# Kernel optimization log

Measured on AMD Instinct MI355X. Metric: run time of the kernel, lower is better.

## Reference

```python
import jax, jax.numpy as jnp
import numpy as np

N_NODES = 30000
N_EDGES = 480000
IN_CH, NF, OUT_CH = 64, 128, 3
N_HIDDEN = 6  # GCN(num_layers=7): conv0 (in->nf) + 6 convs (nf->nf)
SLOPE = 0.02


def setup_inputs() -> dict:
    key = jax.random.key(0)
    ks = jax.random.split(key, 8)
    x = jax.random.normal(ks[0], (N_NODES, IN_CH), dtype=jnp.float32)
    edge_index = jax.random.randint(ks[1], (2, N_EDGES), 0, N_NODES, dtype=jnp.int64)
    W0 = jax.random.normal(ks[2], (IN_CH, NF), dtype=jnp.float32) * (1.0 / np.sqrt(IN_CH))
    b0 = jnp.zeros((NF,), dtype=jnp.float32)
    Wh = jax.random.normal(ks[3], (N_HIDDEN, NF, NF), dtype=jnp.float32) * (1.0 / np.sqrt(NF))
    bh = jnp.zeros((N_HIDDEN, NF), dtype=jnp.float32)
    Wout = jax.random.normal(ks[4], (NF, OUT_CH), dtype=jnp.float32) * (1.0 / np.sqrt(NF))
    bout = jnp.zeros((OUT_CH,), dtype=jnp.float32)
    return {"x": x, "edge_index": edge_index, "W0": W0, "b0": b0,
            "Wh": Wh, "bh": bh, "Wout": Wout, "bout": bout}


def _gcn_norm(edge_index, n):
    # PyG GCNConv default: add self-loops, symmetric normalization D^-1/2 (A+I) D^-1/2
    loop = jnp.arange(n, dtype=edge_index.dtype)
    src = jnp.concatenate([edge_index[0], loop])
    dst = jnp.concatenate([edge_index[1], loop])
    deg = jax.ops.segment_sum(jnp.ones_like(dst, dtype=jnp.float32), dst, num_segments=n)
    dinv = jax.lax.rsqrt(deg)  # deg >= 1 due to self-loops
    norm = dinv[src] * dinv[dst]  # [E+N]
    return src, dst, norm


def _gcn_conv(h, W, b, src, dst, norm, n):
    h = h @ W                                   # [N, F_out]
    msg = h[src] * norm[:, None]                # gather + scale  [E+N, F_out]
    out = jax.ops.segment_sum(msg, dst, num_segments=n)  # scatter-add
    return out + b


def reference(x, edge_index, W0, b0, Wh, bh, Wout, bout):
    n = x.shape[0]
    src, dst, norm = _gcn_norm(edge_index, n)
    # 7-layer GCN stack with LeakyReLU(0.02) between layers; dropout is
    # identity in eval mode (training=False).
    h = _gcn_conv(x, W0, b0, src, dst, norm, n)
    for i in range(N_HIDDEN):
        h = jax.nn.leaky_relu(h, SLOPE)
        h = _gcn_conv(h, Wh[i], bh[i], src, dst, norm, n)
    # outer forward: leaky_relu -> dropout(eval=identity) -> out conv -> tanh*0.5
    h = jax.nn.leaky_relu(h, SLOPE)
    h = _gcn_conv(h, Wout, bout, src, dst, norm, n)
    return jnp.tanh(h) * 0.5
```

## Files before the change

### kernel.cpp

```cpp
#include <hip/hip_runtime.h>
#include <hip/hip_fp16.h>
#include <math.h>

#define NN 30000
#define NE 480000
#define NB 118
#define SCALE 512.0f
#define INVSCALE (1.0f / 512.0f)

typedef _Float16 half8 __attribute__((ext_vector_type(8)));
typedef float floatx4 __attribute__((ext_vector_type(4)));

__device__ __forceinline__ float lrelu(float v) { return v > 0.0f ? v : v * 0.02f; }

__device__ __forceinline__ float4 fma4(float4 v, float w, float4 a) {
    a.x = fmaf(v.x, w, a.x);
    a.y = fmaf(v.y, w, a.y);
    a.z = fmaf(v.z, w, a.z);
    a.w = fmaf(v.w, w, a.w);
    return a;
}

__device__ __forceinline__ float4 loadh4(const __half* p) {
    uint2 raw = *(const uint2*)p;
    float2 f0 = __half22float2(*(__half2*)&raw.x);
    float2 f1 = __half22float2(*(__half2*)&raw.y);
    return make_float4(f0.x, f0.y, f1.x, f1.y);
}

__device__ __forceinline__ void loadh8(const __half* p, float4* lo, float4* hi) {
    uint4 raw = *(const uint4*)p;
    float2 f0 = __half22float2(*(__half2*)&raw.x);
    float2 f1 = __half22float2(*(__half2*)&raw.y);
    float2 f2 = __half22float2(*(__half2*)&raw.z);
    float2 f3 = __half22float2(*(__half2*)&raw.w);
    *lo = make_float4(f0.x, f0.y, f1.x, f1.y);
    *hi = make_float4(f2.x, f2.y, f3.x, f3.y);
}

__device__ __forceinline__ void stnt_h(__half* p, float v) {
    __half hh = __float2half(v);
    __builtin_nontemporal_store(*(_Float16*)&hh, (_Float16*)p);
}


__global__ void k_count(const int* __restrict__ ei, int* __restrict__ cnt,
                        const float* __restrict__ W0, const float* __restrict__ Wh,
                        const float* __restrict__ b0, const float* __restrict__ bh,
                        const float* __restrict__ x,
                        __half* __restrict__ W0t, __half* __restrict__ Wht,
                        float* __restrict__ bs, __half* __restrict__ x16) {
    int g = blockIdx.x * 256 + threadIdx.x;
    if (g < NE) atomicAdd(&cnt[ei[NE + g]], 1);
    {
        float4 v = *(const float4*)&x[(size_t)g * 4];
        __half2 a = __floats2half2_rn(v.x, v.y);
        __half2 b = __floats2half2_rn(v.z, v.w);
        uint2 pk;
        pk.x = *(unsigned int*)&a;
        pk.y = *(unsigned int*)&b;
        *(uint2*)&x16[(size_t)g * 4] = pk;
    }
    if (g < 8192) {
        int k = g >> 7, n = g & 127;
        W0t[n * 64 + k] = __float2half(W0[g] * SCALE);
    } else if (g < 8192 + 98304) {
        int j = g - 8192;
        int l = j >> 14;
        int r = j & 16383;
        int k = r >> 7, n = r & 127;
        Wht[l * 16384 + n * 128 + k] = __float2half(Wh[j]);
    } else if (g < 8192 + 98304 + 896) {
        int j = g - 8192 - 98304;
        bs[j] = (j < 128 ? b0[j] : bh[j - 128]) * SCALE;
    }
}

__global__ void k_scan1(const int* __restrict__ cnt, int* __restrict__ bsum,
                        float* __restrict__ dinv) {
    __shared__ int sd[256];
    int tid = threadIdx.x;
    int i = blockIdx.x * 256 + tid;
    int v = (i < NN) ? cnt[i] : 0;
    if (i < NN) dinv[i] = 1.0f / sqrtf((float)(v + 1));
    sd[tid] = v;
    __syncthreads();
    for (int off = 128; off > 0; off >>= 1) {
        if (tid < off) sd[tid] += sd[tid + off];
        __syncthreads();
    }
    if (tid == 0) bsum[blockIdx.x] = sd[0];
}

__global__ void k_scan3(const int* __restrict__ cnt, const int* __restrict__ bsum,
                        int* __restrict__ row_ptr, int* __restrict__ cursor) {
    __shared__ int sd[256];
    __shared__ int offs[128];
    int tid = threadIdx.x;
    if (tid < 128) offs[tid] = (tid < blockIdx.x) ? bsum[tid] : 0;
    __syncthreads();
    for (int o = 64; o > 0; o >>= 1) {
        if (tid < o) offs[tid] += offs[tid + o];
        __syncthreads();
    }
    int i = blockIdx.x * 256 + tid;
    int v = (i < NN) ? cnt[i] : 0;
    sd[tid] = v;
    __syncthreads();
    for (int off = 1; off < 256; off <<= 1) {
        int t = (tid >= off) ? sd[tid - off] : 0;
        __syncthreads();
        sd[tid] += t;
        __syncthreads();
    }
    if (i < NN) {
        int excl = offs[0] + sd[tid] - v;
        row_ptr[i] = excl;
        cursor[i] = excl;
        if (i == NN - 1) row_ptr[NN] = excl + v;
    }
}

__global__ void k_fill(const int* __restrict__ ei, const float* __restrict__ dinv,
                       int* __restrict__ cursor, int2* __restrict__ csr) {
    int e = blockIdx.x * 256 + threadIdx.x;
    if (e < NE) {
        int s = ei[e];
        int d = ei[NE + e];
        int pos = atomicAdd(&cursor[d], 1);
        float w = dinv[s] * dinv[d];
        csr[pos] = make_int2(s, __float_as_int(w));
    }
}


__launch_bounds__(256)
__global__ void k_layer0(const __half* __restrict__ x, const int* __restrict__ row_ptr,
                         const int2* __restrict__ csr, const float* __restrict__ dinv,
                         const __half* __restrict__ Wt, const float* __restrict__ bias,
                         __half* __restrict__ out16) {
    __shared__ _Float16 hsF[2 * 4 * 16 * 8];
    int tid = threadIdx.x;
    int node0 = blockIdx.x * 16;
    {
        int nl = tid >> 4;
        int node = node0 + nl;
        int c = (tid & 15) * 4;
        float di = dinv[node];
        float w0 = di * di;
        float4 hv = loadh4(&x[(size_t)node * 64 + c]);
        float4 acc[8];
        acc[0] = make_float4(hv.x * w0, hv.y * w0, hv.z * w0, hv.w * w0);
        #pragma unroll
        for (int j = 1; j < 8; j++) acc[j] = make_float4(0.f, 0.f, 0.f, 0.f);
        int e = row_ptr[node];
        int e1 = row_ptr[node + 1];
        for (; e + 8 <= e1; e += 8) {
            int2 sw[8];
            #pragma unroll
            for (int j = 0; j < 8; j++) sw[j] = csr[e + j];
            float4 v[8];
            #pragma unroll
            for (int j = 0; j < 8; j++) v[j] = loadh4(&x[(size_t)sw[j].x * 64 + c]);
            #pragma unroll
            for (int j = 0; j < 8; j++) acc[j] = fma4(v[j], __int_as_float(sw[j].y), acc[j]);
        }
        for (; e < e1; ++e) {
            int2 sw = csr[e];
            float4 v = loadh4(&x[(size_t)sw.x * 64 + c]);
            acc[0] = fma4(v, __int_as_float(sw.y), acc[0]);
        }
        #pragma unroll
        for (int j = 1; j < 8; j++) {
            acc[0].x += acc[j].x;
            acc[0].y += acc[j].y;
            acc[0].z += acc[j].z;
            acc[0].w += acc[j].w;
        }
        int ks = c >> 5, quad = (c >> 3) & 3, jj = c & 7;
        __half2 p0 = __floats2half2_rn(acc[0].x, acc[0].y);
        __half2 p1 = __floats2half2_rn(acc[0].z, acc[0].w);
        uint2 pk;
        pk.x = *(unsigned int*)&p0;
        pk.y = *(unsigned int*)&p1;
        *(uint2*)&hsF[((ks * 4 + quad) * 16 + nl) * 8 + jj] = pk;
    }
    __syncthreads();
    int wave = tid >> 6, lane = tid & 63, quad = lane >> 4, ln = lane & 15;
    half8 afrag[2];
    #pragma unroll
    for (int ks = 0; ks < 2; ks++)
        afrag[ks] = *(const half8*)&hsF[((ks * 4 + quad) * 16 + ln) * 8];
    #pragma unroll
    for (int tc = 0; tc < 2; tc++) {
        int tt = wave + tc * 4;
        floatx4 acc = (floatx4){0.f, 0.f, 0.f, 0.f};
        #pragma unroll
        for (int ks = 0; ks < 2; ks++) {
            half8 b = *(const half8*)&Wt[(size_t)(tt * 16 + ln) * 64 + ks * 32 + quad * 8];
            acc = __builtin_amdgcn_mfma_f32_16x16x32_f16(afrag[ks], b, acc, 0, 0, 0);
        }
        int col = tt * 16 + ln;
        float bb = bias[col];
        #pragma unroll
        for (int r = 0; r < 4; r++) {
            int row = node0 + quad * 4 + r;
            stnt_h(&out16[(size_t)row * 128 + col], lrelu(acc[r] + bb));
        }
    }
}

template <bool LAST>
__launch_bounds__(256)
__global__ void k_layer_h(const __half* __restrict__ h, const int* __restrict__ row_ptr,
                          const int2* __restrict__ csr, const float* __restrict__ dinv,
                          const __half* __restrict__ Wt, const float* __restrict__ bias,
                          __half* __restrict__ out16, const float* __restrict__ Wout,
                          float* __restrict__ u) {
    __shared__ _Float16 hsF[4 * 4 * 16 * 8];
    __shared__ float uacc[4][16][3];
    int tid = threadIdx.x;
    int node0 = blockIdx.x * 16;
    {
        int nl = tid >> 4;
        int node = node0 + nl;
        int c = (tid & 15) * 8;
        float di = dinv[node];
        float w0 = di * di;
        float4 hlo, hhi;
        loadh8(&h[(size_t)node * 128 + c], &hlo, &hhi);
        float4 acc[4][2];
        acc[0][0] = make_float4(hlo.x * w0, hlo.y * w0, hlo.z * w0, hlo.w * w0);
        acc[0][1] = make_float4(hhi.x * w0, hhi.y * w0, hhi.z * w0, hhi.w * w0);
        #pragma unroll
        for (int j = 1; j < 4; j++) {
            acc[j][0] = make_float4(0.f, 0.f, 0.f, 0.f);
            acc[j][1] = make_float4(0.f, 0.f, 0.f, 0.f);
        }
        int e = row_ptr[node];
        int e1 = row_ptr[node + 1];
        for (; e + 4 <= e1; e += 4) {
            int2 sw[4];
            #pragma unroll
            for (int j = 0; j < 4; j++) sw[j] = csr[e + j];
            float4 vlo[4], vhi[4];
            #pragma unroll
            for (int j = 0; j < 4; j++)
                loadh8(&h[(size_t)sw[j].x * 128 + c], &vlo[j], &vhi[j]);
            #pragma unroll
            for (int j = 0; j < 4; j++) {
                float w = __int_as_float(sw[j].y);
                acc[j][0] = fma4(vlo[j], w, acc[j][0]);
                acc[j][1] = fma4(vhi[j], w, acc[j][1]);
            }
        }
        for (; e < e1; ++e) {
            int2 sw = csr[e];
            float4 vlo, vhi;
            loadh8(&h[(size_t)sw.x * 128 + c], &vlo, &vhi);
            float w = __int_as_float(sw.y);
            acc[0][0] = fma4(vlo, w, acc[0][0]);
            acc[0][1] = fma4(vhi, w, acc[0][1]);
        }
        #pragma unroll
        for (int j = 1; j < 4; j++) {
            acc[0][0].x += acc[j][0].x; acc[0][0].y += acc[j][0].y;
            acc[0][0].z += acc[j][0].z; acc[0][0].w += acc[j][0].w;
            acc[0][1].x += acc[j][1].x; acc[0][1].y += acc[j][1].y;
            acc[0][1].z += acc[j][1].z; acc[0][1].w += acc[j][1].w;
        }
        int ks = c >> 5, quad = (c >> 3) & 3;
        __half2 p0 = __floats2half2_rn(acc[0][0].x, acc[0][0].y);
        __half2 p1 = __floats2half2_rn(acc[0][0].z, acc[0][0].w);
        __half2 p2 = __floats2half2_rn(acc[0][1].x, acc[0][1].y);
        __half2 p3 = __floats2half2_rn(acc[0][1].z, acc[0][1].w);
        uint4 pk;
        pk.x = *(unsigned int*)&p0;
        pk.y = *(unsigned int*)&p1;
        pk.z = *(unsigned int*)&p2;
        pk.w = *(unsigned int*)&p3;
        *(uint4*)&hsF[((ks * 4 + quad) * 16 + nl) * 8] = pk;
    }
    __syncthreads();
    int wave = tid >> 6, lane = tid & 63, quad = lane >> 4, ln = lane & 15;
    half8 afrag[4];
    #pragma unroll
    for (int ks = 0; ks < 4; ks++)
        afrag[ks] = *(const half8*)&hsF[((ks * 4 + quad) * 16 + ln) * 8];

    float up[4][3];
    if (LAST) {
        #pragma unroll
        for (int r = 0; r < 4; r++)
            #pragma unroll
            for (int cc = 0; cc < 3; cc++) up[r][cc] = 0.f;
    }

    #pragma unroll
    for (int tc = 0; tc < 2; tc++) {
        int tt = wave + tc * 4;
        floatx4 acc = (floatx4){0.f, 0.f, 0.f, 0.f};
        #pragma unroll
        for (int ks = 0; ks < 4; ks++) {
            half8 b = *(const half8*)&Wt[(size_t)(tt * 16 + ln) * 128 + ks * 32 + quad * 8];
            acc = __builtin_amdgcn_mfma_f32_16x16x32_f16(afrag[ks], b, acc, 0, 0, 0);
        }
        int col = tt * 16 + ln;
        float bb = bias[col];
        if (LAST) {
            float w0o = Wout[col * 3 + 0];
            float w1o = Wout[col * 3 + 1];
            float w2o = Wout[col * 3 + 2];
            #pragma unroll
            for (int r = 0; r < 4; r++) {
                float hv = __half2float(__float2half(lrelu(acc[r] + bb)));
                up[r][0] = fmaf(hv, w0o, up[r][0]);
                up[r][1] = fmaf(hv, w1o, up[r][1]);
                up[r][2] = fmaf(hv, w2o, up[r][2]);
            }
        } else {
            #pragma unroll
            for (int r = 0; r < 4; r++) {
                int row = node0 + quad * 4 + r;
                stnt_h(&out16[(size_t)row * 128 + col], lrelu(acc[r] + bb));
            }
        }
    }

    if (LAST) {
        #pragma unroll
        for (int m = 1; m < 16; m <<= 1) {
            #pragma unroll
            for (int r = 0; r < 4; r++) {
                #pragma unroll
                for (int cc = 0; cc < 3; cc++)
                    up[r][cc] += __shfl_xor(up[r][cc], m);
            }
        }
        if (ln == 0) {
            #pragma unroll
            for (int r = 0; r < 4; r++) {
                #pragma unroll
                for (int cc = 0; cc < 3; cc++)
                    uacc[wave][quad * 4 + r][cc] = up[r][cc];
            }
        }
        __syncthreads();
        if (tid < 48) {
            int row = tid / 3, cc = tid % 3;
            float s = (uacc[0][row][cc] + uacc[1][row][cc]) +
                      (uacc[2][row][cc] + uacc[3][row][cc]);
            u[(size_t)(node0 + row) * 3 + cc] = s;
        }
    }
}


__global__ void k_agg_out(const float* __restrict__ u, const int* __restrict__ row_ptr,
                          const int2* __restrict__ csr, const float* __restrict__ dinv,
                          const float* __restrict__ bout, float* __restrict__ out) {
    int node = blockIdx.x * 256 + threadIdx.x;
    if (node >= NN) return;
    float di = dinv[node], w0 = di * di;
    float s0 = u[(size_t)node * 3 + 0] * w0;
    float s1 = u[(size_t)node * 3 + 1] * w0;
    float s2 = u[(size_t)node * 3 + 2] * w0;
    float b0a = 0.f, b1a = 0.f, b2a = 0.f;
    int e = row_ptr[node];
    int e1 = row_ptr[node + 1];
    for (; e + 2 <= e1; e += 2) {
        int2 swa = csr[e], swb = csr[e + 1];
        float wa = __int_as_float(swa.y), wb = __int_as_float(swb.y);
        const float* ua = &u[(size_t)swa.x * 3];
        const float* ub = &u[(size_t)swb.x * 3];
        s0 = fmaf(ua[0], wa, s0);
        s1 = fmaf(ua[1], wa, s1);
        s2 = fmaf(ua[2], wa, s2);
        b0a = fmaf(ub[0], wb, b0a);
        b1a = fmaf(ub[1], wb, b1a);
        b2a = fmaf(ub[2], wb, b2a);
    }
    for (; e < e1; ++e) {
        int2 sw = csr[e];
        float w = __int_as_float(sw.y);
        const float* us = &u[(size_t)sw.x * 3];
        s0 = fmaf(us[0], w, s0);
        s1 = fmaf(us[1], w, s1);
        s2 = fmaf(us[2], w, s2);
    }
    out[(size_t)node * 3 + 0] = tanhf((s0 + b0a) * INVSCALE + bout[0]) * 0.5f;
    out[(size_t)node * 3 + 1] = tanhf((s1 + b1a) * INVSCALE + bout[1]) * 0.5f;
    out[(size_t)node * 3 + 2] = tanhf((s2 + b2a) * INVSCALE + bout[2]) * 0.5f;
}


extern "C" void kernel_launch(void* const* d_in, const int* in_sizes, int n_in,
                              void* d_out, int out_size, void* d_ws, size_t ws_size,
                              hipStream_t stream) {
    const float* x        = (const float*)d_in[0];
    const int*   ei       = (const int*)d_in[1];
    const float* W0       = (const float*)d_in[2];
    const float* b0       = (const float*)d_in[3];
    const float* Wh       = (const float*)d_in[4];
    const float* bh       = (const float*)d_in[5];
    const float* Wout     = (const float*)d_in[6];
    const float* bout     = (const float*)d_in[7];
    float* out            = (float*)d_out;

    char* ws = (char*)d_ws;
    float*  bufA   = (float*)(ws + 0);
    __half* bufB16 = (__half*)(ws + 15360000);
    __half* bufC16 = (__half*)(ws + 23040000);
    __half* x16    = (__half*)(ws + 30720000);
    __half* W0t16  = (__half*)(ws + 34560000);
    __half* Wht16  = (__half*)(ws + 34576384);
    float*  bs     = (float*)(ws + 34772992);
    float*  dinv   = (float*)(ws + 34776576);
    int*    cnt    = (int*)  (ws + 34896576);
    int*    row_ptr= (int*)  (ws + 35016576);
    int*    cursor = (int*)  (ws + 35136640);
    int2*   csr    = (int2*) (ws + 35256640);

    int* bsum = (int*)bufA;

    hipMemsetAsync(cnt, 0, NN * sizeof(int), stream);
    k_count<<<(NE + 255) / 256, 256, 0, stream>>>(ei, cnt, W0, Wh, b0, bh, x,
                                                  W0t16, Wht16, bs, x16);
    k_scan1<<<NB, 256, 0, stream>>>(cnt, bsum, dinv);
    k_scan3<<<NB, 256, 0, stream>>>(cnt, bsum, row_ptr, cursor);
    k_fill<<<(NE + 255) / 256, 256, 0, stream>>>(ei, dinv, cursor, csr);

    k_layer0<<<NN / 16, 256, 0, stream>>>(x16, row_ptr, csr, dinv, W0t16, bs, bufB16);

    __half* hin = bufB16;
    __half* hout = bufC16;
    for (int i = 0; i < 5; i++) {
        k_layer_h<false><<<NN / 16, 256, 0, stream>>>(hin, row_ptr, csr, dinv,
                                                      Wht16 + (size_t)i * 16384,
                                                      bs + 128 + (size_t)i * 128, hout,
                                                      Wout, bufA);
        __half* t = hin; hin = hout; hout = t;
    }
    k_layer_h<true><<<NN / 16, 256, 0, stream>>>(hin, row_ptr, csr, dinv,
                                                 Wht16 + (size_t)5 * 16384,
                                                 bs + 128 + (size_t)5 * 128, hout,
                                                 Wout, bufA );

    k_agg_out<<<(NN + 255) / 256, 256, 0, stream>>>(bufA, row_ptr, csr, dinv, bout, out);
}
```

Baseline: 316.5 us.

## Sort nodes by degree via counting-sort permutation to balance aggregation work

Builds a 64-bin in-degree histogram and a counting-sort permutation of nodes. Each layer kernel and the output aggregation then process nodes in degree order, so the 16 nodes in a block have similar edge counts and threads in a wave diverge less. The cost is an extra indirection through perm on reads and writes, scattered output stores, a serial single-thread prefix over 64 bins in scan3, and global atomics in scan1 and fill. Indexing u, out16 and out through perm keeps results in original node order.

After: 469.3 us. 48.3% more time.

```diff
diff --git a/kernel.cpp b/kernel.cpp
--- a/kernel.cpp
+++ b/kernel.cpp
@@ -77,12 +77,15 @@
 }
 
 __global__ void k_scan1(const int* __restrict__ cnt, int* __restrict__ bsum,
-                        float* __restrict__ dinv) {
+                        float* __restrict__ dinv, int* __restrict__ hist) {
     __shared__ int sd[256];
     int tid = threadIdx.x;
     int i = blockIdx.x * 256 + tid;
     int v = (i < NN) ? cnt[i] : 0;
-    if (i < NN) dinv[i] = 1.0f / sqrtf((float)(v + 1));
+    if (i < NN) {
+        dinv[i] = 1.0f / sqrtf((float)(v + 1));
+        atomicAdd(&hist[v < 63 ? v : 63], 1);
+    }
     sd[tid] = v;
     __syncthreads();
     for (int off = 128; off > 0; off >>= 1) {
@@ -93,7 +96,12 @@
 }
 
 __global__ void k_scan3(const int* __restrict__ cnt, const int* __restrict__ bsum,
-                        int* __restrict__ row_ptr, int* __restrict__ cursor) {
+                        int* __restrict__ row_ptr, int* __restrict__ cursor,
+                        const int* __restrict__ hist, int* __restrict__ cursor2) {
+    if (blockIdx.x == 0 && threadIdx.x == 0) {
+        int run = 0;
+        for (int d = 0; d < 64; d++) { cursor2[d] = run; run += hist[d]; }
+    }
     __shared__ int sd[256];
     __shared__ int offs[128];
     int tid = threadIdx.x;
@@ -122,7 +130,9 @@
 }
 
 __global__ void k_fill(const int* __restrict__ ei, const float* __restrict__ dinv,
-                       int* __restrict__ cursor, int2* __restrict__ csr) {
+                       int* __restrict__ cursor, int2* __restrict__ csr,
+                       const int* __restrict__ cnt, int* __restrict__ cursor2,
+                       int* __restrict__ perm) {
     int e = blockIdx.x * 256 + threadIdx.x;
     if (e < NE) {
         int s = ei[e];
@@ -131,6 +141,11 @@
         float w = dinv[s] * dinv[d];
         csr[pos] = make_int2(s, __float_as_int(w));
     }
+    if (e < NN) {
+        int dg = cnt[e];
+        int p = atomicAdd(&cursor2[dg < 63 ? dg : 63], 1);
+        perm[p] = e;
+    }
 }
 
 
@@ -138,13 +153,13 @@
 __global__ void k_layer0(const __half* __restrict__ x, const int* __restrict__ row_ptr,
                          const int2* __restrict__ csr, const float* __restrict__ dinv,
                          const __half* __restrict__ Wt, const float* __restrict__ bias,
-                         __half* __restrict__ out16) {
+                         __half* __restrict__ out16, const int* __restrict__ perm) {
     __shared__ _Float16 hsF[2 * 4 * 16 * 8];
     int tid = threadIdx.x;
     int node0 = blockIdx.x * 16;
     {
         int nl = tid >> 4;
-        int node = node0 + nl;
+        int node = perm[node0 + nl];
         int c = (tid & 15) * 4;
         float di = dinv[node];
         float w0 = di * di;
@@ -191,6 +206,9 @@
     #pragma unroll
     for (int ks = 0; ks < 2; ks++)
         afrag[ks] = *(const half8*)&hsF[((ks * 4 + quad) * 16 + ln) * 8];
+    int rn[4];
+    #pragma unroll
+    for (int r = 0; r < 4; r++) rn[r] = perm[node0 + quad * 4 + r];
     #pragma unroll
     for (int tc = 0; tc < 2; tc++) {
         int tt = wave + tc * 4;
@@ -203,10 +221,8 @@
         int col = tt * 16 + ln;
         float bb = bias[col];
         #pragma unroll
-        for (int r = 0; r < 4; r++) {
-            int row = node0 + quad * 4 + r;
-            stnt_h(&out16[(size_t)row * 128 + col], lrelu(acc[r] + bb));
-        }
+        for (int r = 0; r < 4; r++)
+            stnt_h(&out16[(size_t)rn[r] * 128 + col], lrelu(acc[r] + bb));
     }
 }
 
@@ -216,14 +232,14 @@
                           const int2* __restrict__ csr, const float* __restrict__ dinv,
                           const __half* __restrict__ Wt, const float* __restrict__ bias,
                           __half* __restrict__ out16, const float* __restrict__ Wout,
-                          float* __restrict__ u) {
+                          float* __restrict__ u, const int* __restrict__ perm) {
     __shared__ _Float16 hsF[4 * 4 * 16 * 8];
     __shared__ float uacc[4][16][3];
     int tid = threadIdx.x;
     int node0 = blockIdx.x * 16;
     {
         int nl = tid >> 4;
-        int node = node0 + nl;
+        int node = perm[node0 + nl];
         int c = (tid & 15) * 8;
         float di = dinv[node];
         float w0 = di * di;
@@ -295,6 +311,9 @@
             #pragma unroll
             for (int cc = 0; cc < 3; cc++) up[r][cc] = 0.f;
     }
+    int rn[4];
+    #pragma unroll
+    for (int r = 0; r < 4; r++) rn[r] = perm[node0 + quad * 4 + r];
 
     #pragma unroll
     for (int tc = 0; tc < 2; tc++) {
@@ -320,10 +339,8 @@
             }
         } else {
             #pragma unroll
-            for (int r = 0; r < 4; r++) {
-                int row = node0 + quad * 4 + r;
-                stnt_h(&out16[(size_t)row * 128 + col], lrelu(acc[r] + bb));
-            }
+            for (int r = 0; r < 4; r++)
+                stnt_h(&out16[(size_t)rn[r] * 128 + col], lrelu(acc[r] + bb));
         }
     }
 
@@ -350,7 +367,7 @@
             int row = tid / 3, cc = tid % 3;
             float s = (uacc[0][row][cc] + uacc[1][row][cc]) +
                       (uacc[2][row][cc] + uacc[3][row][cc]);
-            u[(size_t)(node0 + row) * 3 + cc] = s;
+            u[(size_t)perm[node0 + row] * 3 + cc] = s;
         }
     }
 }
@@ -358,9 +375,11 @@
 
 __global__ void k_agg_out(const float* __restrict__ u, const int* __restrict__ row_ptr,
                           const int2* __restrict__ csr, const float* __restrict__ dinv,
-                          const float* __restrict__ bout, float* __restrict__ out) {
-    int node = blockIdx.x * 256 + threadIdx.x;
-    if (node >= NN) return;
+                          const float* __restrict__ bout, float* __restrict__ out,
+                          const int* __restrict__ perm) {
+    int g = blockIdx.x * 256 + threadIdx.x;
+    if (g >= NN) return;
+    int node = perm[g];
     float di = dinv[node], w0 = di * di;
     float s0 = u[(size_t)node * 3 + 0] * w0;
     float s1 = u[(size_t)node * 3 + 1] * w0;
@@ -420,17 +439,21 @@
     int*    row_ptr= (int*)  (ws + 35016576);
     int*    cursor = (int*)  (ws + 35136640);
     int2*   csr    = (int2*) (ws + 35256640);
+    int*    perm   = (int*)  (ws + 39096640);
+    int*    hist   = (int*)  (ws + 39216640);
+    int*    cursor2= (int*)  (ws + 39216896);
 
     int* bsum = (int*)bufA;
 
     hipMemsetAsync(cnt, 0, NN * sizeof(int), stream);
+    hipMemsetAsync(hist, 0, 64 * sizeof(int), stream);
     k_count<<<(NE + 255) / 256, 256, 0, stream>>>(ei, cnt, W0, Wh, b0, bh, x,
                                                   W0t16, Wht16, bs, x16);
-    k_scan1<<<NB, 256, 0, stream>>>(cnt, bsum, dinv);
-    k_scan3<<<NB, 256, 0, stream>>>(cnt, bsum, row_ptr, cursor);
-    k_fill<<<(NE + 255) / 256, 256, 0, stream>>>(ei, dinv, cursor, csr);
-
-    k_layer0<<<NN / 16, 256, 0, stream>>>(x16, row_ptr, csr, dinv, W0t16, bs, bufB16);
+    k_scan1<<<NB, 256, 0, stream>>>(cnt, bsum, dinv, hist);
+    k_scan3<<<NB, 256, 0, stream>>>(cnt, bsum, row_ptr, cursor, hist, cursor2);
+    k_fill<<<(NE + 255) / 256, 256, 0, stream>>>(ei, dinv, cursor, csr, cnt, cursor2, perm);
+
+    k_layer0<<<NN / 16, 256, 0, stream>>>(x16, row_ptr, csr, dinv, W0t16, bs, bufB16, perm);
 
     __half* hin = bufB16;
     __half* hout = bufC16;
@@ -438,13 +461,13 @@
         k_layer_h<false><<<NN / 16, 256, 0, stream>>>(hin, row_ptr, csr, dinv,
                                                       Wht16 + (size_t)i * 16384,
                                                       bs + 128 + (size_t)i * 128, hout,
-                                                      Wout, bufA);
+                                                      Wout, bufA, perm);
         __half* t = hin; hin = hout; hout = t;
     }
     k_layer_h<true><<<NN / 16, 256, 0, stream>>>(hin, row_ptr, csr, dinv,
                                                  Wht16 + (size_t)5 * 16384,
                                                  bs + 128 + (size_t)5 * 128, hout,
-                                                 Wout, bufA );
-
-    k_agg_out<<<(NN + 255) / 256, 256, 0, stream>>>(bufA, row_ptr, csr, dinv, bout, out);
-}
+                                                 Wout, bufA , perm);
+
+    k_agg_out<<<(NN + 255) / 256, 256, 0, stream>>>(bufA, row_ptr, csr, dinv, bout, out, perm);
+}
```
